# Kernel tuning notes

Measured on AMD Instinct MI355X. Metric: run time of the kernel, lower is better.

Reference implementation:

```python
import jax, jax.numpy as jnp
import numpy as np

B, N, E, DIN, DOUT = 4, 10000, 320000, 128, 128
EPS = 1e-5


def setup_inputs() -> dict:
    key = jax.random.key(0)
    ks = jax.random.split(key, 10)
    x = jax.random.normal(ks[0], (B, N, DIN), dtype=jnp.float32)
    edge_index = jax.random.randint(ks[1], (2, E), 0, N, dtype=jnp.int64)
    norm = jax.random.uniform(ks[2], (E, 1), dtype=jnp.float32)
    W_w = jax.random.normal(ks[3], (DOUT, DIN), dtype=jnp.float32) / np.sqrt(DIN)
    W_b = jax.random.normal(ks[4], (DOUT,), dtype=jnp.float32) * 0.01
    bn_gamma = jnp.ones((N,), dtype=jnp.float32)
    bn_beta = jnp.zeros((N,), dtype=jnp.float32)
    bn_mean = jax.random.normal(ks[5], (N,), dtype=jnp.float32) * 0.01
    bn_var = jax.random.uniform(ks[6], (N,), dtype=jnp.float32, minval=0.5, maxval=1.5)
    return {"x": x, "edge_index": edge_index, "norm": norm, "W_w": W_w,
            "W_b": W_b, "bn_gamma": bn_gamma, "bn_beta": bn_beta,
            "bn_mean": bn_mean, "bn_var": bn_var}


def reference(x, edge_index, norm, W_w, W_b, bn_gamma, bn_beta, bn_mean, bn_var):
    # Dropout is identity in eval mode.
    h = jnp.einsum('bnf,of->bno', x, W_w) + W_b            # [B, N, DOUT]
    # BatchNorm1d over channel dim = node dim (eval mode, running stats)
    inv = jax.lax.rsqrt(bn_var + EPS)
    h = (h - bn_mean[None, :, None]) * (inv * bn_gamma)[None, :, None] + bn_beta[None, :, None]
    h = jax.nn.gelu(h, approximate=False)                  # torch GELU default = exact erf
    # gather -> scale -> scatter-add message passing
    msgs = h[:, edge_index[1], :] * norm                   # [B, E, DOUT]
    out = jnp.zeros_like(h).at[:, edge_index[0], :].add(msgs)
    return out
```

## Files before the change

### kernel.cpp

```cpp
#include <hip/hip_runtime.h>
#include <math.h>

#define DIN 128
#define DOUT 128
#define EPS 1e-5f
#define CAP 128

typedef unsigned short ushort_t;
typedef __bf16 bf16x8 __attribute__((ext_vector_type(8)));
typedef float f32x16 __attribute__((ext_vector_type(16)));

__device__ __forceinline__ ushort_t f2bf(float f) {
    union { float f; unsigned int i; } v; v.f = f;
    unsigned int x = v.i;
    unsigned int r = x + 0x7fffu + ((x >> 16) & 1u);
    return (ushort_t)(r >> 16);
}

__global__ __launch_bounds__(256) void gemm_bn_gelu_fill(
    const float* __restrict__ x, const float* __restrict__ W,
    const float* __restrict__ bias, const float* __restrict__ gamma,
    const float* __restrict__ beta, const float* __restrict__ mean,
    const float* __restrict__ var, ushort_t* __restrict__ hb,
    const int* __restrict__ ei, const float* __restrict__ norm,
    int* __restrict__ counts, int2* __restrict__ csr,
    int N, int E)
{
    __shared__ ushort_t Wlds[16384];
    __shared__ ushort_t XH[8192];
    __shared__ float sm_mu[16], sm_sc[16], sm_bt[16];

    const int tid = threadIdx.x;
    const int n0 = blockIdx.x * 16;

    {
        int stride = gridDim.x * blockDim.x;
        for (int e = blockIdx.x * blockDim.x + tid; e < E; e += stride) {
            int dst = ei[e];
            int src = ei[E + e];
            int slot = atomicAdd(&counts[dst], 1);
            if (slot < CAP) {
                int2 v; v.x = src; v.y = __float_as_int(norm[e]);
                csr[(size_t)dst * CAP + slot] = v;
            }
        }
    }

    if (tid < 16) {
        int n = n0 + tid;
        sm_mu[tid] = mean[n];
        sm_sc[tid] = rsqrtf(var[n] + EPS) * gamma[n];
        sm_bt[tid] = beta[n];
    }

#pragma unroll
    for (int it = 0; it < 8; ++it) {
        int tup = tid + it * 256;
        int ct = tup >> 9, kc = (tup >> 6) & 7, l = tup & 63;
        int o = ct * 32 + (l & 31);
        int f = kc * 16 + ((l >> 5) << 3);
        const float4* src = (const float4*)(W + o * 128 + f);
        float4 v0 = src[0], v1 = src[1];
        ushort_t* d = &Wlds[tup * 8];
        d[0] = f2bf(v0.x); d[1] = f2bf(v0.y); d[2] = f2bf(v0.z); d[3] = f2bf(v0.w);
        d[4] = f2bf(v1.x); d[5] = f2bf(v1.y); d[6] = f2bf(v1.z); d[7] = f2bf(v1.w);
    }
#pragma unroll
    for (int it = 0; it < 4; ++it) {
        int tup = tid + it * 256;
        int rt = tup >> 9, kc = (tup >> 6) & 7, l = tup & 63;
        int r = rt * 32 + (l & 31);
        int b = r >> 4, i = r & 15;
        size_t grow = (size_t)b * N + n0 + i;
        int f = kc * 16 + ((l >> 5) << 3);
        const float4* src = (const float4*)(x + grow * 128 + f);
        float4 v0 = src[0], v1 = src[1];
        ushort_t* d = &XH[tup * 8];
        d[0] = f2bf(v0.x); d[1] = f2bf(v0.y); d[2] = f2bf(v0.z); d[3] = f2bf(v0.w);
        d[4] = f2bf(v1.x); d[5] = f2bf(v1.y); d[6] = f2bf(v1.z); d[7] = f2bf(v1.w);
    }
    __syncthreads();

    const int w = tid >> 6;
    const int lane = tid & 63;

    bf16x8 bfr[8];
#pragma unroll
    for (int kc = 0; kc < 8; ++kc)
        bfr[kc] = *(const bf16x8*)&Wlds[(w * 512 + kc * 64 + lane) * 8];

    f32x16 acc0 = {};
    f32x16 acc1 = {};
#pragma unroll
    for (int kc = 0; kc < 8; ++kc) {
        bf16x8 a0 = *(const bf16x8*)&XH[(kc * 64 + lane) * 8];
        bf16x8 a1 = *(const bf16x8*)&XH[(512 * 8) + (kc * 64 + lane) * 8];
        acc0 = __builtin_amdgcn_mfma_f32_32x32x16_bf16(a0, bfr[kc], acc0, 0, 0, 0);
        acc1 = __builtin_amdgcn_mfma_f32_32x32x16_bf16(a1, bfr[kc], acc1, 0, 0, 0);
    }
    __syncthreads();

    const int col = w * 32 + (lane & 31);
    const float bias_c = bias[col];
    const int hi4 = (lane >> 5) * 4;
#pragma unroll
    for (int reg = 0; reg < 8; ++reg) {
        int i0 = (reg & 3) + 8 * (reg >> 2) + hi4;
        float mu = sm_mu[i0], sc = sm_sc[i0], bt = sm_bt[i0];
        float vals[4] = { acc0[reg], acc0[reg + 8], acc1[reg], acc1[reg + 8] };
        ushort4 pk;
        {
            float v = vals[0] + bias_c; v = (v - mu) * sc + bt;
            pk.x = f2bf(0.5f * v * (1.0f + erff(v * 0.70710678118654752f)));
        }
        {
            float v = vals[1] + bias_c; v = (v - mu) * sc + bt;
            pk.y = f2bf(0.5f * v * (1.0f + erff(v * 0.70710678118654752f)));
        }
        {
            float v = vals[2] + bias_c; v = (v - mu) * sc + bt;
            pk.z = f2bf(0.5f * v * (1.0f + erff(v * 0.70710678118654752f)));
        }
        {
            float v = vals[3] + bias_c; v = (v - mu) * sc + bt;
            pk.w = f2bf(0.5f * v * (1.0f + erff(v * 0.70710678118654752f)));
        }
        *(ushort4*)&XH[((i0 << 7) + col) << 2] = pk;
    }
    __syncthreads();

    {
        const float4* s = (const float4*)XH;
        float4* d = (float4*)(hb + (size_t)n0 * 512);
#pragma unroll
        for (int i = tid; i < 1024; i += 256) d[i] = s[i];
    }
}

__device__ __forceinline__ void fma8(float* acc, int4 h, float wgt) {
    union { unsigned int i; float f; } t;
    unsigned int u;
    u = (unsigned int)h.x;
    t.i = u << 16;          acc[0] = fmaf(t.f, wgt, acc[0]);
    t.i = u & 0xffff0000u;  acc[1] = fmaf(t.f, wgt, acc[1]);
    u = (unsigned int)h.y;
    t.i = u << 16;          acc[2] = fmaf(t.f, wgt, acc[2]);
    t.i = u & 0xffff0000u;  acc[3] = fmaf(t.f, wgt, acc[3]);
    u = (unsigned int)h.z;
    t.i = u << 16;          acc[4] = fmaf(t.f, wgt, acc[4]);
    t.i = u & 0xffff0000u;  acc[5] = fmaf(t.f, wgt, acc[5]);
    u = (unsigned int)h.w;
    t.i = u << 16;          acc[6] = fmaf(t.f, wgt, acc[6]);
    t.i = u & 0xffff0000u;  acc[7] = fmaf(t.f, wgt, acc[7]);
}

__global__ __launch_bounds__(256) void gather_kernel(
    const ushort_t* __restrict__ hb, const int* __restrict__ counts,
    const int2* __restrict__ csr, float* __restrict__ out, int N)
{
    const int w = threadIdx.x >> 6;
    const int lane = threadIdx.x & 63;
    const int n = blockIdx.x * 4 + w;
    if (n >= N) return;

    int cnt = counts[n];
    if (cnt > CAP) cnt = CAP;
    const int2* bucket = csr + (size_t)n * CAP;

    float acc[8] = {};
    int base = 0;
    while (base < cnt) {
        int lim = cnt - base;
        if (lim > 64) lim = 64;
        int2 meta = bucket[base + lane];
        int j = 0;
        for (; j + 4 <= lim; j += 4) {
            int   s0 = __builtin_amdgcn_readlane(meta.x, j);
            float w0 = __int_as_float(__builtin_amdgcn_readlane(meta.y, j));
            int   s1 = __builtin_amdgcn_readlane(meta.x, j + 1);
            float w1 = __int_as_float(__builtin_amdgcn_readlane(meta.y, j + 1));
            int   s2 = __builtin_amdgcn_readlane(meta.x, j + 2);
            float w2 = __int_as_float(__builtin_amdgcn_readlane(meta.y, j + 2));
            int   s3 = __builtin_amdgcn_readlane(meta.x, j + 3);
            float w3 = __int_as_float(__builtin_amdgcn_readlane(meta.y, j + 3));
            int4 h0 = *(const int4*)(hb + (size_t)s0 * 512 + lane * 8);
            int4 h1 = *(const int4*)(hb + (size_t)s1 * 512 + lane * 8);
            int4 h2 = *(const int4*)(hb + (size_t)s2 * 512 + lane * 8);
            int4 h3 = *(const int4*)(hb + (size_t)s3 * 512 + lane * 8);
            fma8(acc, h0, w0);
            fma8(acc, h1, w1);
            fma8(acc, h2, w2);
            fma8(acc, h3, w3);
        }
        for (; j < lim; ++j) {
            int   s0 = __builtin_amdgcn_readlane(meta.x, j);
            float w0 = __int_as_float(__builtin_amdgcn_readlane(meta.y, j));
            int4 h0 = *(const int4*)(hb + (size_t)s0 * 512 + lane * 8);
            fma8(acc, h0, w0);
        }
        base += 64;
    }

    const size_t bstride = (size_t)N * DOUT;
    float* op = out + (size_t)n * DOUT + lane * 2;
#pragma unroll
    for (int b = 0; b < 4; ++b) {
        float2 v; v.x = acc[b]; v.y = acc[4 + b];
        *(float2*)(op + b * bstride) = v;
    }
}

extern "C" void kernel_launch(void* const* d_in, const int* in_sizes, int n_in,
                              void* d_out, int out_size, void* d_ws, size_t ws_size,
                              hipStream_t stream)
{
    const float* x     = (const float*)d_in[0];
    const int*   ei    = (const int*)d_in[1];
    const float* norm  = (const float*)d_in[2];
    const float* W_w   = (const float*)d_in[3];
    const float* W_b   = (const float*)d_in[4];
    const float* gamma = (const float*)d_in[5];
    const float* beta  = (const float*)d_in[6];
    const float* mean  = (const float*)d_in[7];
    const float* var   = (const float*)d_in[8];
    float* out = (float*)d_out;

    const int N = in_sizes[5];
    const int E = in_sizes[2];
    const int B = in_sizes[0] / (N * DIN);
    (void)B;

    ushort_t* hb  = (ushort_t*)d_ws;
    int* counts   = (int*)(hb + (size_t)N * 512);
    int2* csr     = (int2*)(counts + N);
    csr = (int2*)(((uintptr_t)csr + 7) & ~(uintptr_t)7);

    hipMemsetAsync(counts, 0, (size_t)N * sizeof(int), stream);

    int gemm_blocks = N / 16;
    gemm_bn_gelu_fill<<<gemm_blocks, 256, 0, stream>>>(
        x, W_w, W_b, gamma, beta, mean, var, hb, ei, norm, counts, csr, N, E);

    gather_kernel<<<(N + 3) / 4, 256, 0, stream>>>(hb, counts, csr, out, N);
}
```

Measured before the change: 154.1 us.

## Split gather into per-batch passes with packed bf16 edge metadata

Changes the intermediate h layout from node-interleaved batches to batch-major planes and launches four gather passes, one per batch. The aim is a per-pass working set of about 2.5 MB of bf16 rows that can stay cache-resident. Each wave now processes four edges at once with 16 lanes per row and combines the partial sums with cross-lane shuffles. Edge metadata is packed into 32 bits (16-bit source index plus bf16 weight), which assumes N fits in 16 bits and lowers weight precision. The cost is three extra kernel launches, metadata re-read per pass, and shuffle reductions.

```diff
diff --git a/kernel.cpp b/kernel.cpp
--- a/kernel.cpp
+++ b/kernel.cpp
@@ -23,11 +23,13 @@
     const float* __restrict__ beta, const float* __restrict__ mean,
     const float* __restrict__ var, ushort_t* __restrict__ hb,
     const int* __restrict__ ei, const float* __restrict__ norm,
-    int* __restrict__ counts, int2* __restrict__ csr,
+    int* __restrict__ counts, unsigned int* __restrict__ csr,
     int N, int E)
 {
-    __shared__ ushort_t Wlds[16384];
-    __shared__ ushort_t XH[8192];
+    __shared__ ushort_t SMEM[16384 + 8192];
+    ushort_t* Wlds = SMEM;
+    ushort_t* XH   = SMEM + 16384;
+    float*    Ho   = (float*)SMEM;
     __shared__ float sm_mu[16], sm_sc[16], sm_bt[16];
 
     const int tid = threadIdx.x;
@@ -39,10 +41,9 @@
             int dst = ei[e];
             int src = ei[E + e];
             int slot = atomicAdd(&counts[dst], 1);
-            if (slot < CAP) {
-                int2 v; v.x = src; v.y = __float_as_int(norm[e]);
-                csr[(size_t)dst * CAP + slot] = v;
-            }
+            if (slot < CAP)
+                csr[(size_t)dst * CAP + slot] =
+                    ((unsigned int)src << 16) | (unsigned int)f2bf(norm[e]);
         }
     }
 
@@ -108,55 +109,31 @@
         int i0 = (reg & 3) + 8 * (reg >> 2) + hi4;
         float mu = sm_mu[i0], sc = sm_sc[i0], bt = sm_bt[i0];
         float vals[4] = { acc0[reg], acc0[reg + 8], acc1[reg], acc1[reg + 8] };
-        ushort4 pk;
-        {
-            float v = vals[0] + bias_c; v = (v - mu) * sc + bt;
-            pk.x = f2bf(0.5f * v * (1.0f + erff(v * 0.70710678118654752f)));
+#pragma unroll
+        for (int b = 0; b < 4; ++b) {
+            float v = vals[b] + bias_c;
+            v = (v - mu) * sc + bt;
+            v = 0.5f * v * (1.0f + erff(v * 0.70710678118654752f));
+            Ho[((b << 4) + i0) * 128 + col] = v;
         }
-        {
-            float v = vals[1] + bias_c; v = (v - mu) * sc + bt;
-            pk.y = f2bf(0.5f * v * (1.0f + erff(v * 0.70710678118654752f)));
-        }
-        {
-            float v = vals[2] + bias_c; v = (v - mu) * sc + bt;
-            pk.z = f2bf(0.5f * v * (1.0f + erff(v * 0.70710678118654752f)));
-        }
-        {
-            float v = vals[3] + bias_c; v = (v - mu) * sc + bt;
-            pk.w = f2bf(0.5f * v * (1.0f + erff(v * 0.70710678118654752f)));
-        }
-        *(ushort4*)&XH[((i0 << 7) + col) << 2] = pk;
     }
     __syncthreads();
 
-    {
-        const float4* s = (const float4*)XH;
-        float4* d = (float4*)(hb + (size_t)n0 * 512);
-#pragma unroll
-        for (int i = tid; i < 1024; i += 256) d[i] = s[i];
-    }
-}
-
-__device__ __forceinline__ void fma8(float* acc, int4 h, float wgt) {
-    union { unsigned int i; float f; } t;
-    unsigned int u;
-    u = (unsigned int)h.x;
-    t.i = u << 16;          acc[0] = fmaf(t.f, wgt, acc[0]);
-    t.i = u & 0xffff0000u;  acc[1] = fmaf(t.f, wgt, acc[1]);
-    u = (unsigned int)h.y;
-    t.i = u << 16;          acc[2] = fmaf(t.f, wgt, acc[2]);
-    t.i = u & 0xffff0000u;  acc[3] = fmaf(t.f, wgt, acc[3]);
-    u = (unsigned int)h.z;
-    t.i = u << 16;          acc[4] = fmaf(t.f, wgt, acc[4]);
-    t.i = u & 0xffff0000u;  acc[5] = fmaf(t.f, wgt, acc[5]);
-    u = (unsigned int)h.w;
-    t.i = u << 16;          acc[6] = fmaf(t.f, wgt, acc[6]);
-    t.i = u & 0xffff0000u;  acc[7] = fmaf(t.f, wgt, acc[7]);
-}
-
-__global__ __launch_bounds__(256) void gather_kernel(
+#pragma unroll
+    for (int it = 0; it < 16; ++it) {
+        int idx = it * 512 + tid * 2;
+        float2 v = *(const float2*)&Ho[idx];
+        unsigned int u = (unsigned int)f2bf(v.x) | ((unsigned int)f2bf(v.y) << 16);
+        int b = idx >> 11;
+        int rem = idx & 2047;
+        *(unsigned int*)(hb + ((size_t)b * N + n0) * 128 + rem) = u;
+    }
+}
+
+__global__ __launch_bounds__(256) void gather_pass(
     const ushort_t* __restrict__ hb, const int* __restrict__ counts,
-    const int2* __restrict__ csr, float* __restrict__ out, int N)
+    const unsigned int* __restrict__ csr, float* __restrict__ out,
+    int N, int b)
 {
     const int w = threadIdx.x >> 6;
     const int lane = threadIdx.x & 63;
@@ -165,48 +142,53 @@
 
     int cnt = counts[n];
     if (cnt > CAP) cnt = CAP;
-    const int2* bucket = csr + (size_t)n * CAP;
+    const unsigned int* bucket = csr + (size_t)n * CAP;
+    const ushort_t* hbb = hb + (size_t)b * N * 128;
+    const int t = lane & 15;
+    const int g = lane >> 4;
 
     float acc[8] = {};
-    int base = 0;
-    while (base < cnt) {
-        int lim = cnt - base;
-        if (lim > 64) lim = 64;
-        int2 meta = bucket[base + lane];
-        int j = 0;
-        for (; j + 4 <= lim; j += 4) {
-            int   s0 = __builtin_amdgcn_readlane(meta.x, j);
-            float w0 = __int_as_float(__builtin_amdgcn_readlane(meta.y, j));
-            int   s1 = __builtin_amdgcn_readlane(meta.x, j + 1);
-            float w1 = __int_as_float(__builtin_amdgcn_readlane(meta.y, j + 1));
-            int   s2 = __builtin_amdgcn_readlane(meta.x, j + 2);
-            float w2 = __int_as_float(__builtin_amdgcn_readlane(meta.y, j + 2));
-            int   s3 = __builtin_amdgcn_readlane(meta.x, j + 3);
-            float w3 = __int_as_float(__builtin_amdgcn_readlane(meta.y, j + 3));
-            int4 h0 = *(const int4*)(hb + (size_t)s0 * 512 + lane * 8);
-            int4 h1 = *(const int4*)(hb + (size_t)s1 * 512 + lane * 8);
-            int4 h2 = *(const int4*)(hb + (size_t)s2 * 512 + lane * 8);
-            int4 h3 = *(const int4*)(hb + (size_t)s3 * 512 + lane * 8);
-            fma8(acc, h0, w0);
-            fma8(acc, h1, w1);
-            fma8(acc, h2, w2);
-            fma8(acc, h3, w3);
+    for (int base = 0; base < cnt; base += 64) {
+        int lim = cnt - base; if (lim > 64) lim = 64;
+        unsigned int meta = bucket[base + lane];
+        int nsub = (lim + 3) >> 2;
+        for (int i = 0; i < nsub; ++i) {
+            int sl = (i << 2) | g;
+            unsigned int m = (unsigned int)__builtin_amdgcn_ds_bpermute(sl << 2, (int)meta);
+            int valid = (sl < lim) ? 1 : 0;
+            int src = valid ? (int)(m >> 16) : 0;
+            union { unsigned int u; float f; } wu;
+            wu.u = valid ? (m << 16) : 0u;
+            int4 hv = *(const int4*)(hbb + (size_t)src * 128 + t * 8);
+            union { unsigned int i; float f; } c;
+            unsigned int uu;
+            uu = (unsigned int)hv.x;
+            c.i = uu << 16;          acc[0] = fmaf(c.f, wu.f, acc[0]);
+            c.i = uu & 0xffff0000u;  acc[1] = fmaf(c.f, wu.f, acc[1]);
+            uu = (unsigned int)hv.y;
+            c.i = uu << 16;          acc[2] = fmaf(c.f, wu.f, acc[2]);
+            c.i = uu & 0xffff0000u;  acc[3] = fmaf(c.f, wu.f, acc[3]);
+            uu = (unsigned int)hv.z;
+            c.i = uu << 16;          acc[4] = fmaf(c.f, wu.f, acc[4]);
+            c.i = uu & 0xffff0000u;  acc[5] = fmaf(c.f, wu.f, acc[5]);
+            uu = (unsigned int)hv.w;
+            c.i = uu << 16;          acc[6] = fmaf(c.f, wu.f, acc[6]);
+            c.i = uu & 0xffff0000u;  acc[7] = fmaf(c.f, wu.f, acc[7]);
         }
-        for (; j < lim; ++j) {
-            int   s0 = __builtin_amdgcn_readlane(meta.x, j);
-            float w0 = __int_as_float(__builtin_amdgcn_readlane(meta.y, j));
-            int4 h0 = *(const int4*)(hb + (size_t)s0 * 512 + lane * 8);
-            fma8(acc, h0, w0);
-        }
-        base += 64;
-    }
-
-    const size_t bstride = (size_t)N * DOUT;
-    float* op = out + (size_t)n * DOUT + lane * 2;
-#pragma unroll
-    for (int b = 0; b < 4; ++b) {
-        float2 v; v.x = acc[b]; v.y = acc[4 + b];
-        *(float2*)(op + b * bstride) = v;
+    }
+
+#pragma unroll
+    for (int k = 0; k < 8; ++k) {
+        acc[k] += __shfl_xor(acc[k], 16);
+        acc[k] += __shfl_xor(acc[k], 32);
+    }
+
+    if (g == 0) {
+        float* op = out + ((size_t)b * N + n) * 128 + t * 8;
+        float4 v0 = { acc[0], acc[1], acc[2], acc[3] };
+        float4 v1 = { acc[4], acc[5], acc[6], acc[7] };
+        *(float4*)op = v0;
+        *((float4*)op + 1) = v1;
     }
 }
 
@@ -227,13 +209,10 @@
 
     const int N = in_sizes[5];
     const int E = in_sizes[2];
-    const int B = in_sizes[0] / (N * DIN);
-    (void)B;
-
-    ushort_t* hb  = (ushort_t*)d_ws;
-    int* counts   = (int*)(hb + (size_t)N * 512);
-    int2* csr     = (int2*)(counts + N);
-    csr = (int2*)(((uintptr_t)csr + 7) & ~(uintptr_t)7);
+
+    ushort_t* hb      = (ushort_t*)d_ws;
+    int* counts       = (int*)(hb + (size_t)4 * N * 128);
+    unsigned int* csr = (unsigned int*)(counts + N);
 
     hipMemsetAsync(counts, 0, (size_t)N * sizeof(int), stream);
 
@@ -241,5 +220,7 @@
     gemm_bn_gelu_fill<<<gemm_blocks, 256, 0, stream>>>(
         x, W_w, W_b, gamma, beta, mean, var, hb, ei, norm, counts, csr, N, E);
 
-    gather_kernel<<<(N + 3) / 4, 256, 0, stream>>>(hb, counts, csr, out, N);
-}
+    int gather_blocks = (N + 3) / 4;
+    for (int b = 0; b < 4; ++b)
+        gather_pass<<<gather_blocks, 256, 0, stream>>>(hb, counts, csr, out, N, b);
+}
```

New measurement: 160.9 us. 4.4% more time.
